# Performance work log

Hardware: AMD Instinct MI355X
Metric: run time of the kernel (lower is better)

## Reference

```python
import jax, jax.numpy as jnp
import numpy as np

K = 7            # involution kernel size
GC = 16          # group_channels (canonical involution)
EPS = 1e-6


def ln_cf(x, w, b):
    # channels_first LayerNorm over channel dim (axis=1), as in ConvNeXt utils
    u = jnp.mean(x, axis=1, keepdims=True)
    s = jnp.mean((x - u) ** 2, axis=1, keepdims=True)
    xn = (x - u) / jnp.sqrt(s + EPS)
    return w[:, None, None] * xn + b[:, None, None]


def gelu(x):
    return jax.nn.gelu(x, approximate=False)  # torch nn.GELU default (erf)


def involution(x, w1, b1, w2, b2):
    # x: (B,C,H,W). Kernel-generating head: 1x1 conv -> ReLU -> 1x1 conv.
    B, C, H, W = x.shape
    G = C // GC
    mid = jnp.einsum('bchw,mc->bmhw', x, w1) + b1[None, :, None, None]
    mid = jax.nn.relu(mid)
    wk = jnp.einsum('bmhw,km->bkhw', mid, w2) + b2[None, :, None, None]
    wk = wk.reshape(B, G, K * K, H, W)  # per-pixel, per-group K*K kernels
    pad = (K - 1) // 2
    xp = jnp.pad(x, ((0, 0), (0, 0), (pad, pad), (pad, pad)))
    out = jnp.zeros((B, G, GC, H, W), dtype=x.dtype)
    # accumulate over the K*K spatial offsets (fixed small loop, no big unfold)
    for idx in range(K * K):
        i, j = divmod(idx, K)
        xs = xp[:, :, i:i + H, j:j + W].reshape(B, G, GC, H, W)
        out = out + wk[:, :, idx][:, :, None] * xs
    return out.reshape(B, C, H, W)


def setup_inputs() -> dict:
    key = jax.random.key(0)
    ks = jax.random.split(key, 8)
    B, C, O, H, Wd = 4, 128, 256, 128, 128
    mid = C // 4
    G = C // GC
    sc = 0.05
    return {
        'x': jax.random.normal(ks[0], (B, C, H, Wd), jnp.float32),
        'w1': jax.random.normal(ks[1], (mid, C), jnp.float32) * sc,
        'b1': jnp.zeros((mid,), jnp.float32),
        'w2': jax.random.normal(ks[2], (K * K * G, mid), jnp.float32) * sc,
        'b2': jnp.zeros((K * K * G,), jnp.float32),
        'ln1_w': jnp.ones((C,), jnp.float32),
        'ln1_b': jnp.zeros((C,), jnp.float32),
        'conv_w': jax.random.normal(ks[3], (O, C), jnp.float32) * sc,
        'ln2_w': jnp.ones((O,), jnp.float32),
        'ln2_b': jnp.zeros((O,), jnp.float32),
        'map_w': jax.random.normal(ks[4], (O, C), jnp.float32) * sc,
        'map_b': jnp.zeros((O,), jnp.float32),
        'ln3_w': jnp.ones((O,), jnp.float32),
        'ln3_b': jnp.zeros((O,), jnp.float32),
    }


def reference(x, w1, b1, w2, b2, ln1_w, ln1_b, conv_w, ln2_w, ln2_b,
              map_w, map_b, ln3_w, ln3_b):
    # invblock: Involution -> LayerNorm(channels_first) -> GELU
    x1 = involution(x, w1, b1, w2, b2)
    x1 = gelu(ln_cf(x1, ln1_w, ln1_b))
    # conv_block: 1x1 conv (no bias) -> LayerNorm
    x1 = ln_cf(jnp.einsum('bchw,oc->bohw', x1, conv_w), ln2_w, ln2_b)
    # mapping (channels differ): 1x1 conv (bias) -> LayerNorm
    xm = jnp.einsum('bchw,oc->bohw', x, map_w) + map_b[None, :, None, None]
    xm = ln_cf(xm, ln3_w, ln3_b)
    return gelu(x1 + xm)
```

## Files before the change

kernel.cpp:

```cpp
#include <hip/hip_runtime.h>

typedef unsigned short ushort_t;
typedef unsigned int uint_t;

#define NB 4
#define NC 128
#define NH 128
#define NW 128
#define NPIX 65536
#define NMID 32
#define NKK 49
#define NK 392
#define NKP 400
#define NO 256
#define LN_EPS 1e-6f

typedef __attribute__((ext_vector_type(8))) short short8;
typedef __attribute__((ext_vector_type(4))) float floatx4;

__device__ __forceinline__ float bf2f(ushort_t u) {
    union { uint_t i; float f; } v; v.i = ((uint_t)u) << 16; return v.f;
}
__device__ __forceinline__ float bf2f_lo(uint_t u) {
    union { uint_t i; float f; } v; v.i = u << 16; return v.f;
}
__device__ __forceinline__ float bf2f_hi(uint_t u) {
    union { uint_t i; float f; } v; v.i = u & 0xffff0000u; return v.f;
}
__device__ __forceinline__ ushort_t f2bf(float f) {
    union { float f; uint_t i; } v; v.f = f;
    uint_t x = v.i;
    uint_t r = (x + 0x7FFFu + ((x >> 16) & 1u)) >> 16;
    return (ushort_t)r;
}
__device__ __forceinline__ float gelu_f(float x) {
    return 0.5f * x * (1.0f + erff(x * 0.70710678118654752f));
}
__device__ __forceinline__ float ldin(const void* p, int i, int isf32) {
    return isf32 ? ((const float*)p)[i] : bf2f(((const ushort_t*)p)[i]);
}
__device__ __forceinline__ void gload_lds16(const void* g, void* l) {
    __builtin_amdgcn_global_load_lds(
        (const __attribute__((address_space(1))) void*)g,
        (__attribute__((address_space(3))) void*)l, 16, 0, 0);
}

__global__ void kdetect(const uint_t* __restrict__ xw, int* __restrict__ flag) {
    int lane = threadIdx.x;
    int cnt = 0;
    for (int j = 0; j < 8; j++) {
        uint_t w = xw[lane * 8 + j];
        uint_t e = (w >> 7) & 0xffu;
        if (e >= 110u && e <= 135u) cnt++;
    }
    for (int d = 1; d < 64; d <<= 1) cnt += __shfl_xor(cnt, d);
    if (lane == 0) flag[0] = (cnt < 256) ? 1 : 0;
}

__global__ void ksentinel(uint_t* __restrict__ out, int nwords) {
    int i = blockIdx.x * 256 + threadIdx.x;
    if (i < nwords) out[i] = 0x40004000u;
}

__global__ __launch_bounds__(256) void ktrans(const void* __restrict__ x,
                                              ushort_t* __restrict__ xT,
                                              const int* __restrict__ flag) {
    int isf32 = flag[0];
    int b = blockIdx.z, h = blockIdx.y;
    int wchunk = blockIdx.x & 1, cchunk = blockIdx.x >> 1;
    int w0 = wchunk << 6, c0 = cchunk << 5;
    __shared__ ushort_t tile[32][66];
    int tx = threadIdx.x & 63, ty = threadIdx.x >> 6;
    for (int r = 0; r < 32; r += 4) {
        int idx = (((b * NC + c0 + r + ty) * NH) + h) * NW + w0 + tx;
        tile[r + ty][tx] = isf32 ? f2bf(((const float*)x)[idx])
                                 : ((const ushort_t*)x)[idx];
    }
    __syncthreads();
    int cc = threadIdx.x & 31, wq = threadIdx.x >> 5;
    for (int pp = 0; pp < 64; pp += 8) {
        int wx = pp + wq;
        xT[((size_t)((b * NH + h) * NW) + w0 + wx) * NC + c0 + cc] = tile[cc][wx];
    }
}

__global__ __launch_bounds__(256) void kprepfrag(const void* w1, const void* w2,
                                                 const void* b1, const void* b2,
                                                 const void* ln1w, const void* ln1b,
                                                 const void* ln2w, const void* ln2b,
                                                 const void* map_b,
                                                 const void* ln3w, const void* ln3b,
                                                 const void* conv_w, const void* map_w,
                                                 const int* __restrict__ flag,
                                                 ushort_t* __restrict__ w1b,
                                                 ushort_t* __restrict__ w2b,
                                                 float* __restrict__ b1f,
                                                 float* __restrict__ b2f,
                                                 float* __restrict__ ln1wf,
                                                 float* __restrict__ ln1bf,
                                                 float* __restrict__ ln2wf,
                                                 float* __restrict__ ln2bf,
                                                 float* __restrict__ mbf,
                                                 float* __restrict__ ln3wf,
                                                 float* __restrict__ ln3bf,
                                                 ushort_t* __restrict__ wfrag) {
    int isf32 = flag[0];
    int bid = blockIdx.x;
    if (bid < 128) {
        int i = bid * 256 + threadIdx.x;
        if (i < NMID * NC) w1b[i] = f2bf(ldin(w1, i, isf32));
        if (i < NKP * NMID) w2b[i] = (i < NK * NMID) ? f2bf(ldin(w2, i, isf32))
                                                     : (ushort_t)0;
        if (i < NMID) b1f[i] = ldin(b1, i, isf32);
        if (i < NKP)  b2f[i] = (i < NK) ? ldin(b2, i, isf32) : 0.f;
        if (i < NC) { ln1wf[i] = ldin(ln1w, i, isf32); ln1bf[i] = ldin(ln1b, i, isf32); }
        if (i < NO) {
            ln2wf[i] = ldin(ln2w, i, isf32); ln2bf[i] = ldin(ln2b, i, isf32);
            mbf[i]   = ldin(map_b, i, isf32);
            ln3wf[i] = ldin(ln3w, i, isf32); ln3bf[i] = ldin(ln3b, i, isf32);
        }
    } else {
        int cid = (bid - 128) * 256 + threadIdx.x;
        int lane = cid & 63, n4 = (cid >> 6) & 15, br = (cid >> 10) & 1, kb = cid >> 11;
        int o = n4 * 16 + (lane & 15);
        int ch0 = kb * 32 + (lane >> 4) * 8;
        const void* src = br ? map_w : conv_w;
        ushort_t* dst = wfrag + (size_t)cid * 8;
#pragma unroll
        for (int j = 0; j < 8; j++)
            dst[j] = f2bf(ldin(src, o * NC + ch0 + j, isf32));
    }
}

__global__ __launch_bounds__(512) void k1f(const ushort_t* __restrict__ xT,
                                           const ushort_t* __restrict__ w1b,
                                           const float* __restrict__ b1f,
                                           const ushort_t* __restrict__ w2b,
                                           const float* __restrict__ b2f,
                                           const float* __restrict__ ln1wf,
                                           const float* __restrict__ ln1bf,
                                           ushort_t* __restrict__ y1) {
    __shared__ ushort_t midbuf[64 * 32];
    __shared__ ushort_t wkstage[NKP * 66];

    int t = threadIdx.x;
    int lane = t & 63;
    int w = __builtin_amdgcn_readfirstlane(t >> 6);
    int l16 = lane & 15, quad = lane >> 4;
    int tileid = blockIdx.x;
    int tilex = tileid & 15, tiley = (tileid >> 4) & 15, b = tileid >> 8;
    int h0 = tiley * 8, w0 = tilex * 8;
    int w4 = w & 3;

    if (w < 4) {
        int lpx = 16 * w + l16;
        int py = lpx >> 3, pxx = lpx & 7;
        const ushort_t* abase = xT + (size_t)((b * NH + h0 + py) * NW + w0 + pxx) * NC + quad * 8;
        floatx4 am0 = (floatx4)0.f, am1 = (floatx4)0.f;
#pragma unroll
        for (int kb = 0; kb < 4; kb++) {
            short8 a   = *(const short8*)(abase + kb * 32);
            short8 b0  = *(const short8*)(w1b + (l16) * NC + kb * 32 + quad * 8);
            short8 b1v = *(const short8*)(w1b + (16 + l16) * NC + kb * 32 + quad * 8);
            am0 = __builtin_amdgcn_mfma_f32_16x16x32_bf16(a, b0, am0, 0, 0, 0);
            am1 = __builtin_amdgcn_mfma_f32_16x16x32_bf16(a, b1v, am1, 0, 0, 0);
        }
        float bia0 = b1f[l16], bia1 = b1f[16 + l16];
#pragma unroll
        for (int r = 0; r < 4; r++) {
            int m = 16 * w + quad * 4 + r;
            midbuf[m * 32 + l16]      = f2bf(fmaxf(am0[r] + bia0, 0.f));
            midbuf[m * 32 + 16 + l16] = f2bf(fmaxf(am1[r] + bia1, 0.f));
        }
    }
    __syncthreads();

    {
        short8 aM = *(const short8*)(midbuf + (16 * w4 + l16) * 32 + quad * 8);
        int nt0 = (w < 4) ? 0 : 13;
        int nt1 = (w < 4) ? 13 : 25;
        for (int nt = nt0; nt < nt1; nt++) {
            int n = nt * 16 + l16;
            short8 bw = *(const short8*)(w2b + n * 32 + quad * 8);
            floatx4 c = __builtin_amdgcn_mfma_f32_16x16x32_bf16(aM, bw, (floatx4)0.f, 0, 0, 0);
            float bias = b2f[n];
#pragma unroll
            for (int r = 0; r < 4; r++)
                wkstage[n * 66 + 16 * w4 + quad * 4 + r] = f2bf(c[r] + bias);
        }
    }
    __syncthreads();

    int px = t >> 3, g = t & 7;
    int hy = px >> 3, hx = px & 7;
    int hh0 = h0 + hy, ww0 = w0 + hx;
    int p = (b * NH + hh0) * NW + ww0;
    const ushort_t* wkcol = wkstage + px;

    float a[16];
#pragma unroll
    for (int j = 0; j < 16; j++) a[j] = 0.f;

#pragma unroll
    for (int dy = -3; dy <= 3; dy++) {
        int hh = hh0 + dy;
        if ((unsigned)hh >= (unsigned)NH) continue;
#pragma unroll
        for (int dx = -3; dx <= 3; dx++) {
            int ww = ww0 + dx;
            if ((unsigned)ww >= (unsigned)NW) continue;
            int tap = (dy + 3) * 7 + (dx + 3);
            float wkv = bf2f(wkcol[(g * NKK + tap) * 66]);
            const uint4* xq = (const uint4*)(xT + (size_t)(p + dy * NW + dx) * NC + g * 16);
            uint4 u0 = xq[0], u1 = xq[1];
            a[0]  = fmaf(wkv, bf2f_lo(u0.x), a[0]);
            a[1]  = fmaf(wkv, bf2f_hi(u0.x), a[1]);
            a[2]  = fmaf(wkv, bf2f_lo(u0.y), a[2]);
            a[3]  = fmaf(wkv, bf2f_hi(u0.y), a[3]);
            a[4]  = fmaf(wkv, bf2f_lo(u0.z), a[4]);
            a[5]  = fmaf(wkv, bf2f_hi(u0.z), a[5]);
            a[6]  = fmaf(wkv, bf2f_lo(u0.w), a[6]);
            a[7]  = fmaf(wkv, bf2f_hi(u0.w), a[7]);
            a[8]  = fmaf(wkv, bf2f_lo(u1.x), a[8]);
            a[9]  = fmaf(wkv, bf2f_hi(u1.x), a[9]);
            a[10] = fmaf(wkv, bf2f_lo(u1.y), a[10]);
            a[11] = fmaf(wkv, bf2f_hi(u1.y), a[11]);
            a[12] = fmaf(wkv, bf2f_lo(u1.z), a[12]);
            a[13] = fmaf(wkv, bf2f_hi(u1.z), a[13]);
            a[14] = fmaf(wkv, bf2f_lo(u1.w), a[14]);
            a[15] = fmaf(wkv, bf2f_hi(u1.w), a[15]);
        }
    }

    float s = 0.f, sq = 0.f;
#pragma unroll
    for (int j = 0; j < 16; j++) { s += a[j]; sq += a[j] * a[j]; }
#pragma unroll
    for (int d = 1; d < 8; d <<= 1) {
        s  += __shfl_xor(s, d);
        sq += __shfl_xor(sq, d);
    }
    float mean = s * (1.0f / NC);
    float var = sq * (1.0f / NC) - mean * mean;
    float rstd = rsqrtf(var + LN_EPS);

    uint_t pk[8];
#pragma unroll
    for (int j = 0; j < 8; j++) {
        int c0 = g * 16 + 2 * j;
        float g0 = gelu_f((a[2 * j] - mean) * rstd * ln1wf[c0] + ln1bf[c0]);
        float g1 = gelu_f((a[2 * j + 1] - mean) * rstd * ln1wf[c0 + 1] + ln1bf[c0 + 1]);
        pk[j] = (uint_t)f2bf(g0) | ((uint_t)f2bf(g1) << 16);
    }
    uint4* dst = (uint4*)(y1 + (size_t)p * NC + g * 16);
    dst[0] = make_uint4(pk[0], pk[1], pk[2], pk[3]);
    dst[1] = make_uint4(pk[4], pk[5], pk[6], pk[7]);
}

__global__ __launch_bounds__(256, 4) void k23(const ushort_t* __restrict__ y1,
                                              const ushort_t* __restrict__ xT,
                                              const ushort_t* __restrict__ wfrag,
                                              const float* __restrict__ mbf,
                                              const float* __restrict__ ln2wf,
                                              const float* __restrict__ ln2bf,
                                              const float* __restrict__ ln3wf,
                                              const float* __restrict__ ln3bf,
                                              void* __restrict__ out,
                                              const int* __restrict__ flag) {
    __shared__ __align__(16) char sbuf[32768];

    int isf32 = flag[0];
    int t = threadIdx.x;
    int lane = t & 63;
    int w = __builtin_amdgcn_readfirstlane(t >> 6);
    int quad = lane >> 4, l16 = lane & 15;
    int pair = w >> 1;
    int oh   = w & 1;

    int P0 = blockIdx.x * 32;
    int pw = P0 + pair * 16;
    const ushort_t* aYp = y1 + (size_t)(pw + l16) * NC + quad * 8;
    const ushort_t* aXp = xT + (size_t)(pw + l16) * NC + quad * 8;

    {
        const ushort_t* gsrc = wfrag + (size_t)(w * 512 + lane) * 8;
        char* ldst = sbuf + (size_t)(w * 512) * 16;
#pragma unroll
        for (int i = 0; i < 8; i++)
            gload_lds16(gsrc + i * 64 * 8, ldst + i * 64 * 16);
    }
    short8 Ay[4], Ax[4];
#pragma unroll
    for (int kb = 0; kb < 4; kb++) {
        Ay[kb] = *(const short8*)(aYp + kb * 32);
        Ax[kb] = *(const short8*)(aXp + kb * 32);
    }
    __syncthreads();

    floatx4 accC[8], accM[8];
#pragma unroll
    for (int j = 0; j < 8; j++) { accC[j] = (floatx4)0.f; accM[j] = (floatx4)0.f; }

#pragma unroll
    for (int kb = 0; kb < 4; kb++) {
        short8 ay = Ay[kb], ax = Ax[kb];
#pragma unroll
        for (int j = 0; j < 8; j++) {
            int n4 = oh * 8 + j;
            short8 bc = *(const short8*)(sbuf + (size_t)(n4 * 64 + lane) * 16);
            short8 bm = *(const short8*)(sbuf + 16384 + (size_t)(n4 * 64 + lane) * 16);
            accC[j] = __builtin_amdgcn_mfma_f32_16x16x32_bf16(ay, bc, accC[j], 0, 0, 0);
            accM[j] = __builtin_amdgcn_mfma_f32_16x16x32_bf16(ax, bm, accM[j], 0, 0, 0);
        }
        __syncthreads();
        if (kb < 3) {
            const ushort_t* gsrc = wfrag + ((size_t)(kb + 1) * 2048 + w * 512 + lane) * 8;
            char* ldst = sbuf + (size_t)(w * 512) * 16;
#pragma unroll
            for (int i = 0; i < 8; i++)
                gload_lds16(gsrc + i * 64 * 8, ldst + i * 64 * 16);
            __syncthreads();
        }
    }

#pragma unroll
    for (int j = 0; j < 8; j++) {
        float mb = mbf[(oh * 8 + j) * 16 + l16];
#pragma unroll
        for (int r = 0; r < 4; r++) accM[j][r] += mb;
    }

    floatx4 s1 = (floatx4)0.f, q1 = (floatx4)0.f, s2 = (floatx4)0.f, q2 = (floatx4)0.f;
#pragma unroll
    for (int j = 0; j < 8; j++)
#pragma unroll
        for (int r = 0; r < 4; r++) {
            float a = accC[j][r], m = accM[j][r];
            s1[r] += a; q1[r] += a * a;
            s2[r] += m; q2[r] += m * m;
        }
#pragma unroll
    for (int d = 1; d < 16; d <<= 1) {
#pragma unroll
        for (int r = 0; r < 4; r++) {
            s1[r] += __shfl_xor(s1[r], d);
            q1[r] += __shfl_xor(q1[r], d);
            s2[r] += __shfl_xor(s2[r], d);
            q2[r] += __shfl_xor(q2[r], d);
        }
    }

    float* sstat = (float*)sbuf;
    if (l16 == 0) {
#pragma unroll
        for (int r = 0; r < 4; r++) {
            float* sp = sstat + (((pair * 2 + oh) * 16) + quad * 4 + r) * 4;
            sp[0] = s1[r]; sp[1] = q1[r]; sp[2] = s2[r]; sp[3] = q2[r];
        }
    }
    __syncthreads();

    floatx4 mn1, rs1, mn2, rs2;
#pragma unroll
    for (int r = 0; r < 4; r++) {
        const float* op = sstat + (((pair * 2 + (oh ^ 1)) * 16) + quad * 4 + r) * 4;
        float S1 = s1[r] + op[0], Q1 = q1[r] + op[1];
        float S2 = s2[r] + op[2], Q2 = q2[r] + op[3];
        mn1[r] = S1 * (1.0f / NO);
        rs1[r] = rsqrtf(Q1 * (1.0f / NO) - mn1[r] * mn1[r] + LN_EPS);
        mn2[r] = S2 * (1.0f / NO);
        rs2[r] = rsqrtf(Q2 * (1.0f / NO) - mn2[r] * mn2[r] + LN_EPS);
    }

    int batch = pw >> 14;
    int plocal = (pw & 16383) + quad * 4;
#pragma unroll
    for (int j = 0; j < 8; j++) {
        int o = (oh * 8 + j) * 16 + l16;
        float l2w = ln2wf[o], l2b = ln2bf[o];
        float l3w = ln3wf[o], l3b = ln3bf[o];
        float4 gv;
        {
            float v1, v2;
            v1 = (accC[j][0] - mn1[0]) * rs1[0] * l2w + l2b;
            v2 = (accM[j][0] - mn2[0]) * rs2[0] * l3w + l3b;
            gv.x = gelu_f(v1 + v2);
            v1 = (accC[j][1] - mn1[1]) * rs1[1] * l2w + l2b;
            v2 = (accM[j][1] - mn2[1]) * rs2[1] * l3w + l3b;
            gv.y = gelu_f(v1 + v2);
            v1 = (accC[j][2] - mn1[2]) * rs1[2] * l2w + l2b;
            v2 = (accM[j][2] - mn2[2]) * rs2[2] * l3w + l3b;
            gv.z = gelu_f(v1 + v2);
            v1 = (accC[j][3] - mn1[3]) * rs1[3] * l2w + l2b;
            v2 = (accM[j][3] - mn2[3]) * rs2[3] * l3w + l3b;
            gv.w = gelu_f(v1 + v2);
        }
        size_t oi = ((size_t)(batch * NO + o) << 14) + plocal;
        if (isf32) {
            *(float4*)((float*)out + oi) = gv;
        } else {
            uint_t p0 = (uint_t)f2bf(gv.x) | ((uint_t)f2bf(gv.y) << 16);
            uint_t p1 = (uint_t)f2bf(gv.z) | ((uint_t)f2bf(gv.w) << 16);
            *(uint2*)((ushort_t*)out + oi) = make_uint2(p0, p1);
        }
    }
}

extern "C" void kernel_launch(void* const* d_in, const int* in_sizes, int n_in,
                              void* d_out, int out_size, void* d_ws, size_t ws_size,
                              hipStream_t stream) {
    const void* x      = d_in[0];
    const void* w1     = d_in[1];
    const void* b1     = d_in[2];
    const void* w2     = d_in[3];
    const void* b2     = d_in[4];
    const void* ln1w   = d_in[5];
    const void* ln1b   = d_in[6];
    const void* conv_w = d_in[7];
    const void* ln2w   = d_in[8];
    const void* ln2b   = d_in[9];
    const void* map_w  = d_in[10];
    const void* map_b  = d_in[11];
    const void* ln3w   = d_in[12];
    const void* ln3b   = d_in[13];

    char* ws = (char*)d_ws;
    ushort_t* xT    = (ushort_t*)(ws);
    ushort_t* y1    = (ushort_t*)(ws + 16777216);
    ushort_t* wfrag = (ushort_t*)(ws + 33554432);
    ushort_t* w1b   = (ushort_t*)(ws + 33685504);
    ushort_t* w2b   = (ushort_t*)(ws + 33693696);
    float*    b1f   = (float*)(ws + 33719296);
    float*    b2f   = (float*)(ws + 33719424);
    float*    ln1wf = (float*)(ws + 33721024);
    float*    ln1bf = (float*)(ws + 33721536);
    float*    mbf   = (float*)(ws + 33722048);
    float*    ln2wf = (float*)(ws + 33723072);
    float*    ln2bf = (float*)(ws + 33724096);
    float*    ln3wf = (float*)(ws + 33725120);
    float*    ln3bf = (float*)(ws + 33726144);
    int*      flag  = (int*)(ws + 33727168);
    const size_t NEED_SMALL = 33727184;

    if (ws_size < NEED_SMALL) {
        int nwords = out_size / 2;
        ksentinel<<<(nwords + 255) / 256, 256, 0, stream>>>((uint_t*)d_out, nwords);
        return;
    }

    kdetect<<<1, 64, 0, stream>>>((const uint_t*)x, flag);
    kprepfrag<<<160, 256, 0, stream>>>(w1, w2, b1, b2, ln1w, ln1b,
                                       ln2w, ln2b, map_b, ln3w, ln3b,
                                       conv_w, map_w, flag,
                                       w1b, w2b, b1f, b2f, ln1wf, ln1bf,
                                       ln2wf, ln2bf, mbf, ln3wf, ln3bf, wfrag);
    ktrans<<<dim3(8, 128, 4), 256, 0, stream>>>(x, xT, flag);
    k1f<<<1024, 512, 0, stream>>>(xT, w1b, b1f, w2b, b2f, ln1wf, ln1bf, y1);
    k23<<<NPIX / 32, 256, 0, stream>>>(y1, xT, wfrag, mbf,
                                       ln2wf, ln2bf, ln3wf, ln3bf, d_out, flag);
}
```

Measured before the change: 223.5 us.

## Stage involution halo tile in LDS and inline dtype sniffing per kernel

The involution stage of k1f now cooperatively loads a 14x14 halo tile of xT (all 128 channels) into shared memory. Each wave then handles one channel group for 64 pixels, with its per-pixel kernel weights held in registers, instead of each thread doing repeated global loads of neighbouring pixels. The LayerNorm reduction moves from shuffles to a shared-memory cross-wave reduction. Separately, the standalone kdetect launch is removed and each kernel re-derives the fp32/bf16 flag from the first input words, trading one launch for some redundant work in every block.

```diff
diff --git a/kernel.cpp b/kernel.cpp
--- a/kernel.cpp
+++ b/kernel.cpp
@@ -45,16 +45,23 @@
         (__attribute__((address_space(3))) void*)l, 16, 0, 0);
 }
 
-__global__ void kdetect(const uint_t* __restrict__ xw, int* __restrict__ flag) {
-    int lane = threadIdx.x;
-    int cnt = 0;
-    for (int j = 0; j < 8; j++) {
-        uint_t w = xw[lane * 8 + j];
-        uint_t e = (w >> 7) & 0xffu;
-        if (e >= 110u && e <= 135u) cnt++;
-    }
-    for (int d = 1; d < 64; d <<= 1) cnt += __shfl_xor(cnt, d);
-    if (lane == 0) flag[0] = (cnt < 256) ? 1 : 0;
+__device__ __forceinline__ int sniff_isf32(const void* x, int* lf) {
+    int t = threadIdx.x;
+    if (t < 64) {
+        const uint_t* xw = (const uint_t*)x;
+        int cnt = 0;
+#pragma unroll
+        for (int j = 0; j < 8; j++) {
+            uint_t wv = xw[t * 8 + j];
+            uint_t e = (wv >> 7) & 0xffu;
+            if (e >= 110u && e <= 135u) cnt++;
+        }
+#pragma unroll
+        for (int d = 1; d < 64; d <<= 1) cnt += __shfl_xor(cnt, d);
+        if (t == 0) *lf = (cnt < 256) ? 1 : 0;
+    }
+    __syncthreads();
+    return *lf;
 }
 
 __global__ void ksentinel(uint_t* __restrict__ out, int nwords) {
@@ -63,13 +70,13 @@
 }
 
 __global__ __launch_bounds__(256) void ktrans(const void* __restrict__ x,
-                                              ushort_t* __restrict__ xT,
-                                              const int* __restrict__ flag) {
-    int isf32 = flag[0];
+                                              ushort_t* __restrict__ xT) {
+    __shared__ ushort_t tile[32][66];
+    __shared__ int lf;
+    int isf32 = sniff_isf32(x, &lf);
     int b = blockIdx.z, h = blockIdx.y;
     int wchunk = blockIdx.x & 1, cchunk = blockIdx.x >> 1;
     int w0 = wchunk << 6, c0 = cchunk << 5;
-    __shared__ ushort_t tile[32][66];
     int tx = threadIdx.x & 63, ty = threadIdx.x >> 6;
     for (int r = 0; r < 32; r += 4) {
         int idx = (((b * NC + c0 + r + ty) * NH) + h) * NW + w0 + tx;
@@ -84,14 +91,14 @@
     }
 }
 
-__global__ __launch_bounds__(256) void kprepfrag(const void* w1, const void* w2,
+__global__ __launch_bounds__(256) void kprepfrag(const void* x,
+                                                 const void* w1, const void* w2,
                                                  const void* b1, const void* b2,
                                                  const void* ln1w, const void* ln1b,
                                                  const void* ln2w, const void* ln2b,
                                                  const void* map_b,
                                                  const void* ln3w, const void* ln3b,
                                                  const void* conv_w, const void* map_w,
-                                                 const int* __restrict__ flag,
                                                  ushort_t* __restrict__ w1b,
                                                  ushort_t* __restrict__ w2b,
                                                  float* __restrict__ b1f,
@@ -104,7 +111,8 @@
                                                  float* __restrict__ ln3wf,
                                                  float* __restrict__ ln3bf,
                                                  ushort_t* __restrict__ wfrag) {
-    int isf32 = flag[0];
+    __shared__ int lf;
+    int isf32 = sniff_isf32(x, &lf);
     int bid = blockIdx.x;
     if (bid < 128) {
         int i = bid * 256 + threadIdx.x;
@@ -140,8 +148,11 @@
                                            const float* __restrict__ ln1wf,
                                            const float* __restrict__ ln1bf,
                                            ushort_t* __restrict__ y1) {
+    __shared__ __align__(16) char smem[52800];
     __shared__ ushort_t midbuf[64 * 32];
-    __shared__ ushort_t wkstage[NKP * 66];
+    ushort_t* wkstage = (ushort_t*)smem;
+    uint4*    x8      = (uint4*)smem;
+    float*    sred    = (float*)smem;
 
     int t = threadIdx.x;
     int lane = t & 63;
@@ -191,73 +202,95 @@
     }
     __syncthreads();
 
-    int px = t >> 3, g = t & 7;
-    int hy = px >> 3, hx = px & 7;
-    int hh0 = h0 + hy, ww0 = w0 + hx;
-    int p = (b * NH + hh0) * NW + ww0;
-    const ushort_t* wkcol = wkstage + px;
-
+    uint_t wkp[25];
+#pragma unroll
+    for (int j = 0; j < 24; j++) {
+        uint_t lo = wkstage[(w * NKK + 2 * j) * 66 + lane];
+        uint_t hi = wkstage[(w * NKK + 2 * j + 1) * 66 + lane];
+        wkp[j] = lo | (hi << 16);
+    }
+    wkp[24] = wkstage[(w * NKK + 48) * 66 + lane];
+    __syncthreads();
+
+    for (int it = 0; it < 7; it++) {
+        int idx = it * 512 + t;
+        if (idx < 3136) {
+            int oct = idx & 15, hp = idx >> 4;
+            int hy = hp / 14, hx = hp - hy * 14;
+            int gh = h0 + hy - 3, gw = w0 + hx - 3;
+            uint4 v = make_uint4(0u, 0u, 0u, 0u);
+            if ((unsigned)gh < (unsigned)NH && (unsigned)gw < (unsigned)NW) {
+                v = *(const uint4*)&xT[(size_t)((b * NH + gh) * NW + gw) * NC + 8 * oct];
+            }
+            x8[oct * 197 + hp] = v;
+        }
+    }
+    __syncthreads();
+
+    int py = lane >> 3, pxx = lane & 7;
+    int base0 = py * 14 + pxx;
     float a[16];
 #pragma unroll
     for (int j = 0; j < 16; j++) a[j] = 0.f;
 
 #pragma unroll
-    for (int dy = -3; dy <= 3; dy++) {
-        int hh = hh0 + dy;
-        if ((unsigned)hh >= (unsigned)NH) continue;
-#pragma unroll
-        for (int dx = -3; dx <= 3; dx++) {
-            int ww = ww0 + dx;
-            if ((unsigned)ww >= (unsigned)NW) continue;
-            int tap = (dy + 3) * 7 + (dx + 3);
-            float wkv = bf2f(wkcol[(g * NKK + tap) * 66]);
-            const uint4* xq = (const uint4*)(xT + (size_t)(p + dy * NW + dx) * NC + g * 16);
-            uint4 u0 = xq[0], u1 = xq[1];
-            a[0]  = fmaf(wkv, bf2f_lo(u0.x), a[0]);
-            a[1]  = fmaf(wkv, bf2f_hi(u0.x), a[1]);
-            a[2]  = fmaf(wkv, bf2f_lo(u0.y), a[2]);
-            a[3]  = fmaf(wkv, bf2f_hi(u0.y), a[3]);
-            a[4]  = fmaf(wkv, bf2f_lo(u0.z), a[4]);
-            a[5]  = fmaf(wkv, bf2f_hi(u0.z), a[5]);
-            a[6]  = fmaf(wkv, bf2f_lo(u0.w), a[6]);
-            a[7]  = fmaf(wkv, bf2f_hi(u0.w), a[7]);
-            a[8]  = fmaf(wkv, bf2f_lo(u1.x), a[8]);
-            a[9]  = fmaf(wkv, bf2f_hi(u1.x), a[9]);
-            a[10] = fmaf(wkv, bf2f_lo(u1.y), a[10]);
-            a[11] = fmaf(wkv, bf2f_hi(u1.y), a[11]);
-            a[12] = fmaf(wkv, bf2f_lo(u1.z), a[12]);
-            a[13] = fmaf(wkv, bf2f_hi(u1.z), a[13]);
-            a[14] = fmaf(wkv, bf2f_lo(u1.w), a[14]);
-            a[15] = fmaf(wkv, bf2f_hi(u1.w), a[15]);
-        }
-    }
+    for (int tap = 0; tap < NKK; tap++) {
+        float wkf = (tap & 1) ? bf2f((ushort_t)(wkp[tap >> 1] >> 16))
+                              : bf2f((ushort_t)(wkp[tap >> 1] & 0xffffu));
+        int xa = base0 + (tap / 7) * 14 + (tap % 7);
+        uint4 u0 = x8[(2 * w) * 197 + xa];
+        uint4 u1 = x8[(2 * w + 1) * 197 + xa];
+        a[0]  = fmaf(wkf, bf2f_lo(u0.x), a[0]);
+        a[1]  = fmaf(wkf, bf2f_hi(u0.x), a[1]);
+        a[2]  = fmaf(wkf, bf2f_lo(u0.y), a[2]);
+        a[3]  = fmaf(wkf, bf2f_hi(u0.y), a[3]);
+        a[4]  = fmaf(wkf, bf2f_lo(u0.z), a[4]);
+        a[5]  = fmaf(wkf, bf2f_hi(u0.z), a[5]);
+        a[6]  = fmaf(wkf, bf2f_lo(u0.w), a[6]);
+        a[7]  = fmaf(wkf, bf2f_hi(u0.w), a[7]);
+        a[8]  = fmaf(wkf, bf2f_lo(u1.x), a[8]);
+        a[9]  = fmaf(wkf, bf2f_hi(u1.x), a[9]);
+        a[10] = fmaf(wkf, bf2f_lo(u1.y), a[10]);
+        a[11] = fmaf(wkf, bf2f_hi(u1.y), a[11]);
+        a[12] = fmaf(wkf, bf2f_lo(u1.z), a[12]);
+        a[13] = fmaf(wkf, bf2f_hi(u1.z), a[13]);
+        a[14] = fmaf(wkf, bf2f_lo(u1.w), a[14]);
+        a[15] = fmaf(wkf, bf2f_hi(u1.w), a[15]);
+    }
+    __syncthreads();
 
     float s = 0.f, sq = 0.f;
 #pragma unroll
     for (int j = 0; j < 16; j++) { s += a[j]; sq += a[j] * a[j]; }
-#pragma unroll
-    for (int d = 1; d < 8; d <<= 1) {
-        s  += __shfl_xor(s, d);
-        sq += __shfl_xor(sq, d);
-    }
-    float mean = s * (1.0f / NC);
-    float var = sq * (1.0f / NC) - mean * mean;
+    sred[(w * 64 + lane) * 2]     = s;
+    sred[(w * 64 + lane) * 2 + 1] = sq;
+    __syncthreads();
+    float ts = 0.f, tq = 0.f;
+#pragma unroll
+    for (int r = 0; r < 8; r++) {
+        ts += sred[(r * 64 + lane) * 2];
+        tq += sred[(r * 64 + lane) * 2 + 1];
+    }
+    float mean = ts * (1.0f / NC);
+    float var = tq * (1.0f / NC) - mean * mean;
     float rstd = rsqrtf(var + LN_EPS);
 
+    int p = (b * NH + h0 + py) * NW + w0 + pxx;
     uint_t pk[8];
 #pragma unroll
     for (int j = 0; j < 8; j++) {
-        int c0 = g * 16 + 2 * j;
+        int c0 = 16 * w + 2 * j;
         float g0 = gelu_f((a[2 * j] - mean) * rstd * ln1wf[c0] + ln1bf[c0]);
         float g1 = gelu_f((a[2 * j + 1] - mean) * rstd * ln1wf[c0 + 1] + ln1bf[c0 + 1]);
         pk[j] = (uint_t)f2bf(g0) | ((uint_t)f2bf(g1) << 16);
     }
-    uint4* dst = (uint4*)(y1 + (size_t)p * NC + g * 16);
+    uint4* dst = (uint4*)(y1 + (size_t)p * NC + 16 * w);
     dst[0] = make_uint4(pk[0], pk[1], pk[2], pk[3]);
     dst[1] = make_uint4(pk[4], pk[5], pk[6], pk[7]);
 }
 
-__global__ __launch_bounds__(256, 4) void k23(const ushort_t* __restrict__ y1,
+__global__ __launch_bounds__(256, 4) void k23(const void* __restrict__ x,
+                                              const ushort_t* __restrict__ y1,
                                               const ushort_t* __restrict__ xT,
                                               const ushort_t* __restrict__ wfrag,
                                               const float* __restrict__ mbf,
@@ -265,11 +298,11 @@
                                               const float* __restrict__ ln2bf,
                                               const float* __restrict__ ln3wf,
                                               const float* __restrict__ ln3bf,
-                                              void* __restrict__ out,
-                                              const int* __restrict__ flag) {
+                                              void* __restrict__ out) {
     __shared__ __align__(16) char sbuf[32768];
-
-    int isf32 = flag[0];
+    __shared__ int lf;
+    int isf32 = sniff_isf32(x, &lf);
+
     int t = threadIdx.x;
     int lane = t & 63;
     int w = __builtin_amdgcn_readfirstlane(t >> 6);
@@ -439,7 +472,6 @@
     float*    ln2bf = (float*)(ws + 33724096);
     float*    ln3wf = (float*)(ws + 33725120);
     float*    ln3bf = (float*)(ws + 33726144);
-    int*      flag  = (int*)(ws + 33727168);
     const size_t NEED_SMALL = 33727184;
 
     if (ws_size < NEED_SMALL) {
@@ -448,14 +480,13 @@
         return;
     }
 
-    kdetect<<<1, 64, 0, stream>>>((const uint_t*)x, flag);
-    kprepfrag<<<160, 256, 0, stream>>>(w1, w2, b1, b2, ln1w, ln1b,
+    kprepfrag<<<160, 256, 0, stream>>>(x, w1, w2, b1, b2, ln1w, ln1b,
                                        ln2w, ln2b, map_b, ln3w, ln3b,
-                                       conv_w, map_w, flag,
+                                       conv_w, map_w,
                                        w1b, w2b, b1f, b2f, ln1wf, ln1bf,
                                        ln2wf, ln2bf, mbf, ln3wf, ln3bf, wfrag);
-    ktrans<<<dim3(8, 128, 4), 256, 0, stream>>>(x, xT, flag);
+    ktrans<<<dim3(8, 128, 4), 256, 0, stream>>>(x, xT);
     k1f<<<1024, 512, 0, stream>>>(xT, w1b, b1f, w2b, b2f, ln1wf, ln1bf, y1);
-    k23<<<NPIX / 32, 256, 0, stream>>>(y1, xT, wfrag, mbf,
-                                       ln2wf, ln2bf, ln3wf, ln3bf, d_out, flag);
-}
+    k23<<<NPIX / 32, 256, 0, stream>>>(x, y1, xT, wfrag, mbf,
+                                       ln2wf, ln2bf, ln3wf, ln3bf, d_out);
+}
```

Result: faster. 206.3 us (-7.7%).
